# Kernel tuning notes

Hardware: AMD Instinct MI355X
Metric: run time of the kernel (lower is better)

Reference implementation:

```python
import jax, jax.numpy as jnp
import numpy as np

DIM = 1152
NUM_HEADS = 16
HEAD_DIM = DIM // NUM_HEADS
EPS = 1e-6
B, N, M = 4, 4096, 512


def setup_inputs() -> dict:
    key = jax.random.key(0)
    ks = jax.random.split(key, 12)
    s = 0.02
    return {
        "x": jax.random.normal(ks[0], (B, N, DIM), dtype=jnp.float32),
        "cond": jax.random.normal(ks[1], (B, M, DIM), dtype=jnp.float32),
        "kv_seqlen": jax.random.randint(ks[2], (B,), 1, M + 1, dtype=jnp.int32),
        "q_w": jax.random.normal(ks[3], (DIM, DIM), dtype=jnp.float32) * s,
        "q_b": jnp.zeros((DIM,), jnp.float32),
        "kv_w": jax.random.normal(ks[4], (DIM, 2 * DIM), dtype=jnp.float32) * s,
        "kv_b": jnp.zeros((2 * DIM,), jnp.float32),
        "proj_w": jax.random.normal(ks[5], (DIM, DIM), dtype=jnp.float32) * s,
        "proj_b": jnp.zeros((DIM,), jnp.float32),
        "qn_w": jnp.ones((HEAD_DIM,), jnp.float32),
        "kn_w": jnp.ones((HEAD_DIM,), jnp.float32),
    }


def _rmsnorm_fp32(t, w):
    # RMSNorm computed in fp32 over head_dim, then cast back
    t32 = t.astype(jnp.float32)
    inv = jax.lax.rsqrt(jnp.mean(t32 * t32, axis=-1, keepdims=True) + EPS)
    return ((t32 * inv) * w.astype(jnp.float32)).astype(t.dtype)


def reference(x, cond, kv_seqlen, q_w, q_b, kv_w, kv_b, proj_w, proj_b, qn_w, kn_w):
    b, n, c = x.shape
    out_dtype = x.dtype
    q = (x @ q_w + q_b).reshape(b, n, NUM_HEADS, HEAD_DIM)           # [B,N,H,D]
    kv = (cond @ kv_w + kv_b).reshape(b, -1, 2, NUM_HEADS, HEAD_DIM)
    k, v = kv[:, :, 0], kv[:, :, 1]                                   # [B,M,H,D]
    q = _rmsnorm_fp32(q, qn_w)
    k = _rmsnorm_fp32(k, kn_w)
    # original casts to bf16 for the attention kernel when out_dtype is fp32
    q16, k16, v16 = q.astype(jnp.bfloat16), k.astype(jnp.bfloat16), v.astype(jnp.bfloat16)
    scale = 1.0 / np.sqrt(HEAD_DIM)
    scores = jnp.einsum("bnhd,bmhd->bhnm", q16, k16,
                        preferred_element_type=jnp.float32) * scale   # [B,H,N,M] fp32
    m = cond.shape[1]
    valid = (jnp.arange(m)[None, :] < kv_seqlen[:, None])             # [B,M] ragged kv mask
    scores = jnp.where(valid[:, None, None, :], scores, -jnp.inf)
    probs = jax.nn.softmax(scores, axis=-1).astype(jnp.bfloat16)
    out = jnp.einsum("bhnm,bmhd->bnhd", probs, v16).reshape(b, n, c)
    out = out.astype(out_dtype)
    return out @ proj_w + proj_b
```

## Files before the change

kernel.cpp:

```cpp
#include <hip/hip_runtime.h>
#include <math.h>

typedef unsigned short ushort_t;
typedef __attribute__((ext_vector_type(4))) float floatx4;
typedef __attribute__((ext_vector_type(8))) short bf16x8;

#define DIMC 1152
#define NHEADS 16
#define HDIM 72

__device__ __forceinline__ ushort_t f2bf(float f) {
  unsigned u = __float_as_uint(f);
  u += 0x7FFFu + ((u >> 16) & 1u);
  return (ushort_t)(u >> 16);
}
__device__ __forceinline__ float bf2f(ushort_t s) {
  return __uint_as_float(((unsigned)s) << 16);
}

__device__ __forceinline__ void gload_lds16(const ushort_t* g, ushort_t* l) {
  __builtin_amdgcn_global_load_lds(
      (const __attribute__((address_space(1))) unsigned int*)(const void*)g,
      (__attribute__((address_space(3))) unsigned int*)(void*)l, 16, 0, 0);
}

__device__ __forceinline__ bf16x8 load_bf16x8(const ushort_t* p) {
  union { bf16x8 v; uint4 u; } t;
  t.u = *(const uint4*)p;
  return t.v;
}

__global__ void prep_kernel(const float* __restrict__ x, ushort_t* __restrict__ x16,
                            const float* __restrict__ cond, ushort_t* __restrict__ cond16,
                            const float* __restrict__ q_w, ushort_t* __restrict__ qwT,
                            const float* __restrict__ kv_w, ushort_t* __restrict__ kvwT,
                            const float* __restrict__ proj_w, ushort_t* __restrict__ pwT) {
  __shared__ ushort_t tile[64 * 80];
  int blk = blockIdx.x;
  int tid = threadIdx.x;

  if (blk < 10368) {
    const float* src; ushort_t* dst; int i;
    if (blk < 9216) { src = x; dst = x16; i = blk * 256 + tid; }
    else            { src = cond; dst = cond16; i = (blk - 9216) * 256 + tid; }
    float4 f0 = ((const float4*)src)[2 * (size_t)i];
    float4 f1 = ((const float4*)src)[2 * (size_t)i + 1];
    union { ushort_t s[8]; uint4 u; } t;
    t.s[0] = f2bf(f0.x); t.s[1] = f2bf(f0.y); t.s[2] = f2bf(f0.z); t.s[3] = f2bf(f0.w);
    t.s[4] = f2bf(f1.x); t.s[5] = f2bf(f1.y); t.s[6] = f2bf(f1.z); t.s[7] = f2bf(f1.w);
    ((uint4*)dst)[i] = t.u;
    return;
  }

  const float* W; ushort_t* Wt; int N, idx;
  if (blk < 10692)      { W = q_w;    Wt = qwT;  N = 1152; idx = blk - 10368; }
  else if (blk < 11340) { W = kv_w;   Wt = kvwT; N = 2304; idx = blk - 10692; }
  else                  { W = proj_w; Wt = pwT;  N = 1152; idx = blk - 11340; }
  const int K = 1152;
  int k0 = (idx % 18) * 64, n0 = (idx / 18) * 64;

  int kl = tid >> 4, n4 = tid & 15;
  for (int rr = 0; rr < 4; rr++) {
    int k = kl + rr * 16;
    float4 f = *(const float4*)(W + (size_t)(k0 + k) * N + n0 + n4 * 4);
    tile[(n4 * 4 + 0) * 80 + k] = f2bf(f.x);
    tile[(n4 * 4 + 1) * 80 + k] = f2bf(f.y);
    tile[(n4 * 4 + 2) * 80 + k] = f2bf(f.z);
    tile[(n4 * 4 + 3) * 80 + k] = f2bf(f.w);
  }
  __syncthreads();
  int nl = tid >> 2, kq = tid & 3;
  uint4 v0 = *(const uint4*)(tile + nl * 80 + kq * 16);
  uint4 v1 = *(const uint4*)(tile + nl * 80 + kq * 16 + 8);
  *(uint4*)(Wt + (size_t)(n0 + nl) * K + k0 + kq * 16) = v0;
  *(uint4*)(Wt + (size_t)(n0 + nl) * K + k0 + kq * 16 + 8) = v1;
}

template <bool OUT_F32>
__global__ __launch_bounds__(256, 2) void gemm128_kernel(
    const ushort_t* __restrict__ A0, const ushort_t* __restrict__ Bt0,
    const float* __restrict__ bias0, void* __restrict__ C0,
    int NTn0, int Ncols0,
    const ushort_t* __restrict__ A1, const ushort_t* __restrict__ Bt1,
    const float* __restrict__ bias1, void* __restrict__ C1,
    int NTn1, int Ncols1,
    int nblk0, int Kdim) {
  __shared__ ushort_t S[32768];

  int lin = blockIdx.x;
  int cpx = gridDim.x >> 3;
  int wg = (lin & 7) * cpx + (lin >> 3);

  const ushort_t* Aseg; const ushort_t* Bseg;
  const float* bias; void* Cptr; int NTn, Ncols;
  if (wg < nblk0) {
    Aseg = A0; Bseg = Bt0; bias = bias0; Cptr = C0; NTn = NTn0; Ncols = Ncols0;
  } else {
    wg -= nblk0;
    Aseg = A1; Bseg = Bt1; bias = bias1; Cptr = C1; NTn = NTn1; Ncols = Ncols1;
  }
  int mt = wg / NTn, nt = wg % NTn;
  int m0 = mt * 128, n0 = nt * 128;

  int tid = threadIdx.x;
  int wid = tid >> 6, lane = tid & 63, quad = lane >> 4, l16 = lane & 15;
  int wr = wid >> 1, wc = wid & 1;
  const int qoff = (quad * 8) ^ ((l16 & 8) << 1);

  const int srow = tid >> 2;
  const int scol = ((tid & 3) * 8) ^ ((tid & 32) ? 16 : 0);
  const ushort_t* Abase = Aseg + (size_t)m0 * Kdim;
  const ushort_t* Bbase = Bseg + (size_t)n0 * Kdim;

  auto stageA = [&](int t, int ks) {
    const ushort_t* src = Abase + (size_t)srow * Kdim + t * 64 + ks * 32 + scol;
    ushort_t* dst = S + (t & 1) * 16384 + ks * 4096 + (tid >> 6) * 512;
    gload_lds16(src, dst);
    gload_lds16(src + (size_t)64 * Kdim, dst + 2048);
  };
  auto stageB = [&](int t, int ks) {
    const ushort_t* src = Bbase + (size_t)srow * Kdim + t * 64 + ks * 32 + scol;
    ushort_t* dst = S + (t & 1) * 16384 + 8192 + ks * 4096 + (tid >> 6) * 512;
    gload_lds16(src, dst);
    gload_lds16(src + (size_t)64 * Kdim, dst + 2048);
  };

  floatx4 zero = {0.f, 0.f, 0.f, 0.f};
  floatx4 acc[4][4];
#pragma unroll
  for (int i = 0; i < 4; i++)
#pragma unroll
    for (int j = 0; j < 4; j++) acc[i][j] = zero;

  int NT = Kdim >> 6;

  stageA(0, 0); stageB(0, 0);
  stageA(0, 1); stageB(0, 1);
  asm volatile("s_waitcnt vmcnt(4)" ::: "memory");
  __builtin_amdgcn_s_barrier();

  for (int t = 0; t < NT; ++t) {
    const int abase = (t & 1) * 16384;
    const int arow = (wr * 64 + l16) * 32 + qoff;
    const int brow = (wc * 64 + l16) * 32 + qoff;

#pragma unroll
    for (int ks = 0; ks < 2; ++ks) {
      const int ab = abase + ks * 4096;
      const int bb = abase + 8192 + ks * 4096;
      bf16x8 af[4], bfr[4];
#pragma unroll
      for (int mf = 0; mf < 4; mf++)
        af[mf] = *(const bf16x8*)(S + ab + arow + mf * 512);
#pragma unroll
      for (int c = 0; c < 4; c++)
        bfr[c] = *(const bf16x8*)(S + bb + brow + c * 512);
      if (t + 1 < NT) { stageA(t + 1, ks); stageB(t + 1, ks); }
      __builtin_amdgcn_s_barrier();
      asm volatile("s_waitcnt lgkmcnt(0)" ::: "memory");
      __builtin_amdgcn_sched_barrier(0);
      __builtin_amdgcn_s_setprio(1);
#pragma unroll
      for (int c = 0; c < 4; c++)
#pragma unroll
        for (int mf = 0; mf < 4; mf++)
          acc[mf][c] = __builtin_amdgcn_mfma_f32_16x16x32_bf16(af[mf], bfr[c], acc[mf][c], 0, 0, 0);
      __builtin_amdgcn_s_setprio(0);
      if (t + 1 < NT)
        asm volatile("s_waitcnt vmcnt(4)" ::: "memory");
      else
        asm volatile("s_waitcnt vmcnt(0)" ::: "memory");
      __builtin_amdgcn_s_barrier();
    }
  }

  float bv[4];
#pragma unroll
  for (int c = 0; c < 4; c++) bv[c] = bias[n0 + wc * 64 + c * 16 + l16];
#pragma unroll
  for (int mf = 0; mf < 4; mf++)
#pragma unroll
    for (int c = 0; c < 4; c++)
#pragma unroll
      for (int r = 0; r < 4; r++) {
        int row = m0 + wr * 64 + mf * 16 + quad * 4 + r;
        int col = n0 + wc * 64 + c * 16 + l16;
        float v = acc[mf][c][r] + bv[c];
        if constexpr (OUT_F32)
          ((float*)Cptr)[(size_t)row * Ncols + col] = v;
        else
          ((ushort_t*)Cptr)[(size_t)row * Ncols + col] = f2bf(v);
      }
}

__global__ void rmsvt_kernel(ushort_t* __restrict__ kv16,
                             const float* __restrict__ kn_w,
                             ushort_t* __restrict__ vT) {
  __shared__ ushort_t tile[64 * 84];
  int blk = blockIdx.x;
  int tid = threadIdx.x;

  if (blk < 8192) {
    int gw = blk * 4 + (tid >> 6);
    int lane = tid & 63;
    int row = gw >> 4, h = gw & 15;
    ushort_t* base = kv16 + (size_t)row * 2304 + h * HDIM;
    float v0 = bf2f(base[lane]);
    float v1 = (lane < 8) ? bf2f(base[64 + lane]) : 0.f;
    float ss = v0 * v0 + v1 * v1;
    for (int off = 1; off < 64; off <<= 1) ss += __shfl_xor(ss, off);
    float inv = rsqrtf(ss / 72.0f + 1e-6f);
    base[lane] = f2bf(v0 * inv * kn_w[lane]);
    if (lane < 8) base[64 + lane] = f2bf(v1 * inv * kn_w[64 + lane]);
    return;
  }

  int idx = blk - 8192;
  int m0 = (idx & 7) * 64, h = (idx >> 3) & 15, b = idx >> 7;
  int row = tid >> 2, sl = tid & 3;
  const ushort_t* src =
      kv16 + (size_t)(b * 512 + m0 + row) * 2304 + DIMC + h * HDIM;
#pragma unroll
  for (int k = 0; k < 5; k++) {
    int s = sl + 4 * k;
    if (s < 18) {
      uint2 v = *(const uint2*)(src + s * 4);
      *(uint2*)(tile + row * 84 + s * 4) = v;
    }
  }
  __syncthreads();
  size_t dbase = (size_t)((b * 16 + h) * 80) * 512 + m0;
#pragma unroll
  for (int it = 0; it < 5; it++) {
    int i2 = it * 256 + tid;
    int d = i2 >> 4, mseg = i2 & 15;
    union { ushort_t s[4]; uint2 u; } pk;
    if (d < HDIM) {
      pk.s[0] = tile[(mseg * 4 + 0) * 84 + d];
      pk.s[1] = tile[(mseg * 4 + 1) * 84 + d];
      pk.s[2] = tile[(mseg * 4 + 2) * 84 + d];
      pk.s[3] = tile[(mseg * 4 + 3) * 84 + d];
    } else {
      ushort_t f = (d == HDIM) ? (ushort_t)0x3F80 : (ushort_t)0;
      pk.s[0] = pk.s[1] = pk.s[2] = pk.s[3] = f;
    }
    *(uint2*)(vT + dbase + (size_t)d * 512 + mseg * 4) = pk.u;
  }
}

__global__ __launch_bounds__(256, 4) void attn_kernel(
    const ushort_t* __restrict__ q16, const ushort_t* __restrict__ kv16,
    const ushort_t* __restrict__ vT, const int* __restrict__ seqlens,
    const float* __restrict__ qn_w, ushort_t* __restrict__ att) {
  __shared__ ushort_t KV[22 * 512];
  __shared__ __align__(16) unsigned Ps[4][32 * 32];
  int b = blockIdx.z, h = blockIdx.y, n0 = blockIdx.x * 128;
  int tid = threadIdx.x, wid = tid >> 6, lane = tid & 63;
  int quad = lane >> 4, l16 = lane & 15;
  int seqlen = seqlens[b];
  const float qscale = 0.11785113019775793f * 1.44269504088896f;

  unsigned* Pw = &Ps[wid][0];
  const int xorm = (l16 & 7) << 2;

  bf16x8 qf[2][3];
  float ssq[2] = {0.f, 0.f};
  for (int rb = 0; rb < 2; rb++)
    for (int ks = 0; ks < 3; ks++) {
      if (ks == 2 && quad > 0) {
        qf[rb][ks] = (bf16x8){0, 0, 0, 0, 0, 0, 0, 0};
      } else {
        size_t off = ((size_t)(b * 4096 + n0 + wid * 32 + rb * 16 + l16)) * DIMC +
                     h * HDIM + ks * 32 + quad * 8;
        qf[rb][ks] = load_bf16x8(q16 + off);
        union { bf16x8 v; ushort_t s[8]; } e;
        e.v = qf[rb][ks];
        for (int j = 0; j < 8; j++) {
          float xv = bf2f(e.s[j]);
          ssq[rb] += xv * xv;
        }
      }
    }
  for (int rb = 0; rb < 2; rb++) {
    ssq[rb] += __shfl_xor(ssq[rb], 16);
    ssq[rb] += __shfl_xor(ssq[rb], 32);
  }
  for (int rb = 0; rb < 2; rb++) {
    float inv = rsqrtf(ssq[rb] / 72.0f + 1e-6f) * qscale;
    for (int ks = 0; ks < 3; ks++) {
      if (ks == 2 && quad > 0) continue;
      float4 w0 = *(const float4*)(qn_w + ks * 32 + quad * 8);
      float4 w1 = *(const float4*)(qn_w + ks * 32 + quad * 8 + 4);
      union { bf16x8 v; ushort_t s[8]; } e;
      e.v = qf[rb][ks];
      e.s[0] = f2bf(bf2f(e.s[0]) * inv * w0.x);
      e.s[1] = f2bf(bf2f(e.s[1]) * inv * w0.y);
      e.s[2] = f2bf(bf2f(e.s[2]) * inv * w0.z);
      e.s[3] = f2bf(bf2f(e.s[3]) * inv * w0.w);
      e.s[4] = f2bf(bf2f(e.s[4]) * inv * w1.x);
      e.s[5] = f2bf(bf2f(e.s[5]) * inv * w1.y);
      e.s[6] = f2bf(bf2f(e.s[6]) * inv * w1.z);
      e.s[7] = f2bf(bf2f(e.s[7]) * inv * w1.w);
      qf[rb][ks] = e.v;
    }
  }

  floatx4 zero = {0.f, 0.f, 0.f, 0.f};
  floatx4 of[2][5];
  for (int rb = 0; rb < 2; rb++)
    for (int nf = 0; nf < 5; nf++) of[rb][nf] = zero;

  const size_t kvrow = (size_t)b * 512;
  const size_t vbase = (size_t)((b * 16 + h) * 80) * 512;

  int ntiles = (seqlen + 63) >> 6;
  for (int mt = 0; mt < ntiles; mt++) {
    int m0 = mt * 64;

    __syncthreads();
    for (int id = wid; id < 22; id += 4) {
      const ushort_t* src;
      if (id < 12) {
        int c = (id * 11) >> 5;
        int ks = id - c * 3;
        src = kv16 + (size_t)(kvrow + m0 + c * 16 + l16) * 2304 + h * HDIM +
              ks * 32 + quad * 8;
      } else {
        int v = id - 12;
        int nf = v >> 1, ks = v & 1;
        src = vT + (vbase + (size_t)(nf * 16 + l16) * 512) + m0 + ks * 32 + quad * 8;
      }
      gload_lds16(src, KV + id * 512);
    }
    __syncthreads();

    floatx4 sf[2][4];
    for (int rb = 0; rb < 2; rb++)
      for (int c = 0; c < 4; c++) sf[rb][c] = zero;
    for (int c = 0; c < 4; c++)
      for (int ks = 0; ks < 3; ks++) {
        bf16x8 kf = *(const bf16x8*)(KV + (c * 3 + ks) * 512 + lane * 8);
        for (int rb = 0; rb < 2; rb++)
          sf[rb][c] = __builtin_amdgcn_mfma_f32_16x16x32_bf16(kf, qf[rb][ks], sf[rb][c], 0, 0, 0);
      }

    bool partial = (m0 + 64) > seqlen;
    for (int rb = 0; rb < 2; rb++) {
      unsigned* prow = Pw + (rb * 16 + l16) * 32;
      for (int c = 0; c < 4; c++) {
        float p0 = __builtin_amdgcn_exp2f(sf[rb][c][0]);
        float p1 = __builtin_amdgcn_exp2f(sf[rb][c][1]);
        float p2 = __builtin_amdgcn_exp2f(sf[rb][c][2]);
        float p3 = __builtin_amdgcn_exp2f(sf[rb][c][3]);
        if (partial) {
          int kabs = m0 + c * 16 + quad * 4;
          p0 = (kabs < seqlen) ? p0 : 0.f;
          p1 = (kabs + 1 < seqlen) ? p1 : 0.f;
          p2 = (kabs + 2 < seqlen) ? p2 : 0.f;
          p3 = (kabs + 3 < seqlen) ? p3 : 0.f;
        }
        unsigned w0, w1;
        asm("v_cvt_pk_bf16_f32 %0, %1, %2" : "=v"(w0) : "v"(p0), "v"(p1));
        asm("v_cvt_pk_bf16_f32 %0, %1, %2" : "=v"(w1) : "v"(p2), "v"(p3));
        uint2 pw2; pw2.x = w0; pw2.y = w1;
        *(uint2*)(prow + ((8 * c + 2 * quad) ^ xorm)) = pw2;
      }
    }

    for (int ks = 0; ks < 2; ks++) {
      bf16x8 pf[2];
      for (int rb = 0; rb < 2; rb++) {
        const unsigned* prow = Pw + (rb * 16 + l16) * 32;
        pf[rb] = *(const bf16x8*)(prow + ((ks * 16 + quad * 4) ^ xorm));
      }
      for (int nf = 0; nf < 5; nf++) {
        bf16x8 vf = *(const bf16x8*)(KV + (12 + nf * 2 + ks) * 512 + lane * 8);
        for (int rb = 0; rb < 2; rb++)
          of[rb][nf] = __builtin_amdgcn_mfma_f32_16x16x32_bf16(pf[rb], vf, of[rb][nf], 0, 0, 0);
      }
    }
  }

  for (int rb = 0; rb < 2; rb++) {
    float invl[4];
    for (int r = 0; r < 4; r++) {
      float lsum = __shfl(of[rb][4][r], (lane & 48) | 8);
      invl[r] = 1.0f / lsum;
    }
    for (int nf = 0; nf < 5; nf++) {
      int d = nf * 16 + l16;
      if (d < HDIM) {
        for (int r = 0; r < 4; r++) {
          size_t o = ((size_t)(b * 4096 + n0 + wid * 32 + rb * 16 + quad * 4 + r)) * DIMC +
                     h * HDIM + d;
          att[o] = f2bf(of[rb][nf][r] * invl[r]);
        }
      }
    }
  }
}

extern "C" void kernel_launch(void* const* d_in, const int* in_sizes, int n_in,
                              void* d_out, int out_size, void* d_ws, size_t ws_size,
                              hipStream_t stream) {
  const float* x      = (const float*)d_in[0];
  const float* cond   = (const float*)d_in[1];
  const int*   seqlen = (const int*)d_in[2];
  const float* q_w    = (const float*)d_in[3];
  const float* q_b    = (const float*)d_in[4];
  const float* kv_w   = (const float*)d_in[5];
  const float* kv_b   = (const float*)d_in[6];
  const float* proj_w = (const float*)d_in[7];
  const float* proj_b = (const float*)d_in[8];
  const float* qn_w   = (const float*)d_in[9];
  const float* kn_w   = (const float*)d_in[10];
  float* out = (float*)d_out;

  char* ws = (char*)d_ws;
  size_t o = 0;
  ushort_t* qwT    = (ushort_t*)(ws + o); o += (size_t)1152 * 1152 * 2;
  ushort_t* kvwT   = (ushort_t*)(ws + o); o += (size_t)2304 * 1152 * 2;
  ushort_t* pwT    = (ushort_t*)(ws + o); o += (size_t)1152 * 1152 * 2;
  ushort_t* q16    = (ushort_t*)(ws + o); o += (size_t)16384 * 1152 * 2;
  ushort_t* kv16   = (ushort_t*)(ws + o); o += (size_t)2048 * 2304 * 2;
  ushort_t* vT     = (ushort_t*)(ws + o); o += (size_t)64 * 80 * 512 * 2;
  ushort_t* att    = (ushort_t*)(ws + o); o += (size_t)16384 * 1152 * 2;
  ushort_t* x16    = (ushort_t*)(ws + o); o += (size_t)16384 * 1152 * 2;
  ushort_t* cond16 = (ushort_t*)(ws + o); o += (size_t)2048 * 1152 * 2;

  dim3 blk(256);

  prep_kernel<<<dim3(11664), blk, 0, stream>>>(
      x, x16, cond, cond16, q_w, qwT, kv_w, kvwT, proj_w, pwT);

  gemm128_kernel<false><<<dim3(1152 + 288), blk, 0, stream>>>(
      x16, qwT, q_b, q16, 9, 1152,
      cond16, kvwT, kv_b, kv16, 18, 2304,
      1152, 1152);

  rmsvt_kernel<<<dim3(8192 + 512), blk, 0, stream>>>(kv16, kn_w, vT);

  attn_kernel<<<dim3(32, 16, 4), blk, 0, stream>>>(q16, kv16, vT, seqlen, qn_w, att);

  gemm128_kernel<true><<<dim3(1152), blk, 0, stream>>>(
      att, pwT, proj_b, out, 9, 1152,
      att, pwT, proj_b, out, 9, 1152,
      1152, 1152);
}
```

Baseline: 360.2 us.

## Register-prefetch next KV tile to overlap global loads with attention compute

Replaces the synchronous direct-to-LDS loads of each K/V tile with a register double-buffer. The next tile is loaded into registers while the current tile is computed, then written to LDS at the start of the next iteration. Per-slot base addresses and strides are precomputed outside the loop. This hides global memory latency behind the MFMA and softmax work, at the cost of extra VGPRs and an explicit vmcnt wait before each LDS store.

```diff
diff --git a/kernel.cpp b/kernel.cpp
--- a/kernel.cpp
+++ b/kernel.cpp
@@ -313,26 +313,57 @@
   const size_t kvrow = (size_t)b * 512;
   const size_t vbase = (size_t)((b * 16 + h) * 80) * 512;
 
+  const ushort_t* sbase[6];
+  int sstep[6];
+#pragma unroll
+  for (int j = 0; j < 6; j++) {
+    int id = wid + j * 4;
+    if (id < 22) {
+      if (id < 12) {
+        int c = (id * 11) >> 5, ks = id - c * 3;
+        sbase[j] = kv16 + (size_t)(kvrow + c * 16 + l16) * 2304 + h * HDIM +
+                   ks * 32 + quad * 8;
+        sstep[j] = 64 * 2304;
+      } else {
+        int v = id - 12, nf = v >> 1, ks = v & 1;
+        sbase[j] = vT + vbase + (size_t)(nf * 16 + l16) * 512 + ks * 32 + quad * 8;
+        sstep[j] = 64;
+      }
+    } else {
+      sbase[j] = kv16; sstep[j] = 0;
+    }
+  }
+
   int ntiles = (seqlen + 63) >> 6;
+
+  uint4 kvreg[6];
+#pragma unroll
+  for (int j = 0; j < 6; j++) {
+    int id = wid + j * 4;
+    if (id < 22) kvreg[j] = *(const uint4*)(sbase[j]);
+  }
+
   for (int mt = 0; mt < ntiles; mt++) {
+    asm volatile("s_waitcnt vmcnt(0)" ::: "memory");
+    __builtin_amdgcn_s_barrier();
+#pragma unroll
+    for (int j = 0; j < 6; j++) {
+      int id = wid + j * 4;
+      if (id < 22) *(uint4*)(KV + id * 512 + lane * 8) = kvreg[j];
+    }
+    if (mt + 1 < ntiles) {
+#pragma unroll
+      for (int j = 0; j < 6; j++) {
+        int id = wid + j * 4;
+        if (id < 22)
+          kvreg[j] = *(const uint4*)(sbase[j] + (size_t)(mt + 1) * sstep[j]);
+      }
+    }
+    asm volatile("s_waitcnt lgkmcnt(0)" ::: "memory");
+    __builtin_amdgcn_s_barrier();
+    __builtin_amdgcn_sched_barrier(0);
+
     int m0 = mt * 64;
-
-    __syncthreads();
-    for (int id = wid; id < 22; id += 4) {
-      const ushort_t* src;
-      if (id < 12) {
-        int c = (id * 11) >> 5;
-        int ks = id - c * 3;
-        src = kv16 + (size_t)(kvrow + m0 + c * 16 + l16) * 2304 + h * HDIM +
-              ks * 32 + quad * 8;
-      } else {
-        int v = id - 12;
-        int nf = v >> 1, ks = v & 1;
-        src = vT + (vbase + (size_t)(nf * 16 + l16) * 512) + m0 + ks * 32 + quad * 8;
-      }
-      gload_lds16(src, KV + id * 512);
-    }
-    __syncthreads();
 
     floatx4 sf[2][4];
     for (int rb = 0; rb < 2; rb++)
```

Result: slower. 455.6 us (+26.5%).
